# Kernel optimization log

Hardware: AMD Instinct MI355X
Metric: run time of the kernel (lower is better)

## Reference

```python
import jax, jax.numpy as jnp
import numpy as np

L = 2048  # sequence length
V = 2048  # num_tokens == channel width (one-hot embedding)
B = 4     # batch


def _pos_bias(v_table):
    # pos[i,j] = max(i-j, 0); embed via [L,1] table -> [L,L]
    i = jnp.arange(L)
    pos = jnp.maximum(i[:, None] - i[None, :], 0)
    return v_table[pos, 0]


def setup_inputs() -> dict:
    key = jax.random.key(0)
    ks = jax.random.split(key, 11)
    idx = jax.random.randint(ks[0], (B, L), 0, V)
    lin = lambda k, std: (jax.random.normal(k, (V, V), dtype=jnp.float32) * std)
    return {
        "idx": idx,
        # layer_zero: all std=1 (explicit re-init in torch code)
        "Wq0": lin(ks[1], 1.0), "Wk0": lin(ks[2], 1.0), "Wv0": lin(ks[3], 1.0),
        # layer_one: Wk std=1 (re-init), Wv std=0.02 (default init); Wq is zero-fn
        "Wk1": lin(ks[4], 1.0), "Wv1": lin(ks[5], 0.02),
        # layer_two: Wq,Wv std=1 (re-init), Wk std=0.02 (default)
        "Wq2": lin(ks[6], 1.0), "Wk2": lin(ks[7], 0.02), "Wv2": lin(ks[8], 1.0),
        # relative-position embedding tables [L,1], std=0.02
        "v0": jax.random.normal(ks[9], (L, 1), dtype=jnp.float32) * 0.02,
        "v1": jax.random.normal(ks[10], (L, 1), dtype=jnp.float32) * 0.02,
    }


def reference(idx, Wq0, Wk0, Wv0, Wk1, Wv1, Wq2, Wk2, Wv2, v0, v1):
    e = jax.nn.one_hot(idx, V, dtype=jnp.float32)            # [B,L,V]
    tril = jnp.tril(jnp.ones((L, L), dtype=bool))
    p0 = _pos_bias(v0)                                       # [L,L]
    p1 = _pos_bias(v1)

    # layer_zero(e, e): scores = Q@K^T + sum_e(K)[:,None]*pos, tril, @V (no softmax)
    K0 = e @ Wk0.T
    Q0 = e @ Wq0.T
    V0 = e @ Wv0.T
    s0 = jnp.einsum('bqv,bkv->bqk', Q0, K0) + K0.sum(-1)[:, :, None] * p0[None]
    l0 = jnp.where(tril, s0, 0.0) @ V0                       # [B,L,V]

    # layer_one(l0, e): Wq is zero-fn -> only the pos-bias term survives
    K1 = e @ Wk1.T
    V1 = l0 @ Wv1.T
    s1 = K1.sum(-1)[:, :, None] * p1[None]
    l1 = jnp.where(tril, s1, 0.0) @ V1

    # layer_two(e, l1): v is zero-fn -> no pos bias
    K2 = l1 @ Wk2.T
    Q2 = e @ Wq2.T
    V2 = e @ Wv2.T
    s2 = jnp.einsum('bqv,bkv->bqk', Q2, K2)
    logits = jnp.where(tril, s2, 0.0) @ V2                   # [B,L,V]
    return logits
```

## Files before the change

kernel.cpp:

```cpp
#include <hip/hip_runtime.h>

typedef float f32x4 __attribute__((ext_vector_type(4)));
typedef short s16x8 __attribute__((ext_vector_type(8)));

constexpr int L = 2048;
constexpr int V = 2048;
constexpr int NB = 4;
constexpr size_t VV  = (size_t)V * V;
constexpr size_t BLV = (size_t)NB * L * V;
constexpr size_t LV  = (size_t)L * V;

__device__ __forceinline__ unsigned short f2bf(float f) {
    unsigned u = __float_as_uint(f);
    u = (u + 0x7FFFu + ((u >> 16) & 1u)) >> 16;
    return (unsigned short)u;
}
__device__ __forceinline__ float bf2f(unsigned short s) {
    return __uint_as_float(((unsigned)s) << 16);
}

__device__ __forceinline__ void gload16(const unsigned short* g, unsigned short* l) {
    auto gp = (const __attribute__((address_space(1))) unsigned int*)g;
    auto lp = (__attribute__((address_space(3))) unsigned int*)l;
    __builtin_amdgcn_global_load_lds(gp, lp, 16, 0, 0);
}

#define SBAR __builtin_amdgcn_sched_barrier(0)


__device__ __forceinline__ void stage_half(const unsigned short* G, int r0, int k0, int s,
                                           unsigned short* slice, int wave, int lane) {
    int rl = lane >> 2, slot = lane & 3;
    #pragma unroll
    for (int r = 0; r < 2; ++r) {
        int rowl = r * 128 + wave * 16 + rl;
        int colg = k0 + s * 32 + ((slot ^ ((rowl >> 1) & 3)) * 8);
        gload16(G + (size_t)(r0 + rowl) * 2048 + colg,
                slice + (size_t)(r * 128 + wave * 16) * 32);
    }
}

__device__ __forceinline__ s16x8 frag64(const unsigned short* slice, int row, int kc) {
    return *(const s16x8*)&slice[row * 32 + ((kc ^ ((row >> 1) & 3)) * 8)];
}

__device__ __forceinline__ void kloop64(const unsigned short* Ab, const unsigned short* Bb,
                                        int m0, int n0, int NT, unsigned short* lds,
                                        int wave, int lane, int wr, int wc,
                                        f32x4 (&acc)[8][4]) {
    const int r15 = lane & 15, kc = lane >> 4;

    stage_half(Ab, m0, 0, 0, lds + 0,     wave, lane);
    stage_half(Bb, n0, 0, 0, lds + 16384, wave, lane);
    stage_half(Ab, m0, 0, 1, lds + 8192,  wave, lane);
    stage_half(Bb, n0, 0, 1, lds + 24576, wave, lane);
    asm volatile("s_waitcnt vmcnt(4)" ::: "memory");
    SBAR; __builtin_amdgcn_s_barrier(); SBAR;

    for (int t = 0; t < NT; ++t) {
        unsigned short* cur = lds + (t & 1) * 32768;
        unsigned short* nxt = lds + ((t + 1) & 1) * 32768;
        const bool pre = (t + 1 < NT);
        const int k1 = (t + 1) * 64;

        s16x8 b0[4], b1[4], a[4];

        #pragma unroll
        for (int nf = 0; nf < 4; ++nf)
            b0[nf] = frag64(cur + 16384, wc * 64 + nf * 16 + r15, kc);
        #pragma unroll
        for (int mf = 0; mf < 4; ++mf)
            a[mf] = frag64(cur, wr * 128 + mf * 16 + r15, kc);
        if (pre) stage_half(Ab, m0, k1, 0, nxt, wave, lane);
        SBAR; __builtin_amdgcn_s_barrier(); SBAR;
        __builtin_amdgcn_s_setprio(1);
        #pragma unroll
        for (int mf = 0; mf < 4; ++mf)
            #pragma unroll
            for (int nf = 0; nf < 4; ++nf)
                acc[mf][nf] = __builtin_amdgcn_mfma_f32_16x16x32_bf16(a[mf], b0[nf], acc[mf][nf], 0, 0, 0);
        __builtin_amdgcn_s_setprio(0);
        SBAR; __builtin_amdgcn_s_barrier(); SBAR;

        #pragma unroll
        for (int mf = 0; mf < 4; ++mf)
            a[mf] = frag64(cur, wr * 128 + (mf + 4) * 16 + r15, kc);
        if (pre) stage_half(Bb, n0, k1, 0, nxt + 16384, wave, lane);
        SBAR; __builtin_amdgcn_s_barrier(); SBAR;
        __builtin_amdgcn_s_setprio(1);
        #pragma unroll
        for (int mf = 0; mf < 4; ++mf)
            #pragma unroll
            for (int nf = 0; nf < 4; ++nf)
                acc[mf + 4][nf] = __builtin_amdgcn_mfma_f32_16x16x32_bf16(a[mf], b0[nf], acc[mf + 4][nf], 0, 0, 0);
        __builtin_amdgcn_s_setprio(0);
        SBAR;
        if (pre) { asm volatile("s_waitcnt vmcnt(4)" ::: "memory"); }
        else     { asm volatile("s_waitcnt vmcnt(0)" ::: "memory"); }
        SBAR; __builtin_amdgcn_s_barrier(); SBAR;

        #pragma unroll
        for (int nf = 0; nf < 4; ++nf)
            b1[nf] = frag64(cur + 24576, wc * 64 + nf * 16 + r15, kc);
        #pragma unroll
        for (int mf = 0; mf < 4; ++mf)
            a[mf] = frag64(cur + 8192, wr * 128 + mf * 16 + r15, kc);
        if (pre) stage_half(Ab, m0, k1, 1, nxt + 8192, wave, lane);
        SBAR; __builtin_amdgcn_s_barrier(); SBAR;
        __builtin_amdgcn_s_setprio(1);
        #pragma unroll
        for (int mf = 0; mf < 4; ++mf)
            #pragma unroll
            for (int nf = 0; nf < 4; ++nf)
                acc[mf][nf] = __builtin_amdgcn_mfma_f32_16x16x32_bf16(a[mf], b1[nf], acc[mf][nf], 0, 0, 0);
        __builtin_amdgcn_s_setprio(0);
        SBAR; __builtin_amdgcn_s_barrier(); SBAR;

        #pragma unroll
        for (int mf = 0; mf < 4; ++mf)
            a[mf] = frag64(cur + 8192, wr * 128 + (mf + 4) * 16 + r15, kc);
        if (pre) stage_half(Bb, n0, k1, 1, nxt + 24576, wave, lane);
        SBAR; __builtin_amdgcn_s_barrier(); SBAR;
        __builtin_amdgcn_s_setprio(1);
        #pragma unroll
        for (int mf = 0; mf < 4; ++mf)
            #pragma unroll
            for (int nf = 0; nf < 4; ++nf)
                acc[mf + 4][nf] = __builtin_amdgcn_mfma_f32_16x16x32_bf16(a[mf], b1[nf], acc[mf + 4][nf], 0, 0, 0);
        __builtin_amdgcn_s_setprio(0);
        SBAR;
        if (pre) { asm volatile("s_waitcnt vmcnt(4)" ::: "memory"); }
        SBAR; __builtin_amdgcn_s_barrier(); SBAR;
    }
}

template<int OUTM, bool TOEP>
__global__ __launch_bounds__(512, 2) void gemm_big(
    const unsigned short* __restrict__ A, size_t sA,
    const unsigned short* __restrict__ B, size_t sB,
    float* __restrict__ outF, unsigned short* __restrict__ outH, size_t sO,
    const int* __restrict__ idxp, const float* __restrict__ ks)
{
    __shared__ __align__(16) unsigned short lds[2 * 32768];

    const int tid  = threadIdx.x;
    const int lane = tid & 63, wave = tid >> 6;
    const int wr = wave >> 2, wc = wave & 3;
    const int bz = blockIdx.z;
    int bx = blockIdx.x, by = blockIdx.y;
    if constexpr (TOEP) { int tswap = bx; bx = by; by = tswap; }
    const int m0 = by * 256, n0 = bx * 256;
    const int r15 = lane & 15, kc = lane >> 4;

    const unsigned short* Ab = A + (size_t)bz * sA;
    const unsigned short* Bb = B + (size_t)bz * sB;
    const int NT = TOEP ? 4 * (bx + 1) : 32;

    f32x4 acc[8][4];
    const f32x4 zf = {0.f, 0.f, 0.f, 0.f};
    #pragma unroll
    for (int i = 0; i < 8; ++i)
        #pragma unroll
        for (int j = 0; j < 4; ++j) acc[i][j] = zf;

    kloop64(Ab, Bb, m0, n0, NT, lds, wave, lane, wr, wc, acc);

    float csc[4];
    if constexpr (TOEP) {
        #pragma unroll
        for (int nf = 0; nf < 4; ++nf) {
            int gcol = n0 + wc * 64 + nf * 16 + r15;
            csc[nf] = ks[idxp[bz * L + gcol]];
        }
    }
    #pragma unroll
    for (int mf = 0; mf < 8; ++mf) {
        #pragma unroll
        for (int r = 0; r < 4; ++r) {
            int grow = m0 + wr * 128 + mf * 16 + kc * 4 + r;
            #pragma unroll
            for (int nf = 0; nf < 4; ++nf) {
                float v = acc[mf][nf][r];
                if constexpr (TOEP) v *= csc[nf];
                int gcol = n0 + wc * 64 + nf * 16 + r15;
                size_t o = (size_t)bz * sO + (size_t)grow * 2048 + gcol;
                if constexpr (OUTM == 0) outF[o] = v;
                else                     outH[o] = f2bf(v);
            }
        }
    }
}

struct PDesc { const unsigned short* A; const unsigned short* B; float* oF; unsigned short* oH; };

__global__ __launch_bounds__(512, 2) void gemm_pre_big(PDesc d0, PDesc d1, PDesc d2) {
    PDesc d = (blockIdx.z == 0) ? d0 : (blockIdx.z == 1) ? d1 : d2;
    __shared__ __align__(16) unsigned short lds[2 * 32768];

    const int tid  = threadIdx.x;
    const int lane = tid & 63, wave = tid >> 6;
    const int wr = wave >> 2, wc = wave & 3;
    const int m0 = blockIdx.y * 256, n0 = blockIdx.x * 256;
    const int r15 = lane & 15, kc = lane >> 4;

    f32x4 acc[8][4];
    const f32x4 zf = {0.f, 0.f, 0.f, 0.f};
    #pragma unroll
    for (int i = 0; i < 8; ++i)
        #pragma unroll
        for (int j = 0; j < 4; ++j) acc[i][j] = zf;

    kloop64(d.A, d.B, m0, n0, 32, lds, wave, lane, wr, wc, acc);

    const bool isF = (d.oF != nullptr);
    #pragma unroll
    for (int mf = 0; mf < 8; ++mf) {
        #pragma unroll
        for (int r = 0; r < 4; ++r) {
            int grow = m0 + wr * 128 + mf * 16 + kc * 4 + r;
            #pragma unroll
            for (int nf = 0; nf < 4; ++nf) {
                float v = acc[mf][nf][r];
                int gcol = n0 + wc * 64 + nf * 16 + r15;
                size_t o = (size_t)grow * 2048 + gcol;
                if (isF) d.oF[o] = v;
                else     d.oH[o] = f2bf(v);
            }
        }
    }
}

__global__ __launch_bounds__(512, 2) void gemm_preK(const unsigned short* __restrict__ A,
                                                    const unsigned short* __restrict__ B,
                                                    float* __restrict__ outP) {
    __shared__ __align__(16) unsigned short lds[2 * 32768];

    const int tid  = threadIdx.x;
    const int lane = tid & 63, wave = tid >> 6;
    const int wr = wave >> 2, wc = wave & 3;
    const int m0 = blockIdx.y * 256, n0 = blockIdx.x * 256;
    const int r15 = lane & 15, kc = lane >> 4;
    const int z = blockIdx.z;

    const unsigned short* Ab = A + z * 512;
    const unsigned short* Bb = B + z * 512;
    float* outF = outP + (size_t)z * VV;

    f32x4 acc[8][4];
    const f32x4 zf = {0.f, 0.f, 0.f, 0.f};
    #pragma unroll
    for (int i = 0; i < 8; ++i)
        #pragma unroll
        for (int j = 0; j < 4; ++j) acc[i][j] = zf;

    kloop64(Ab, Bb, m0, n0, 8, lds, wave, lane, wr, wc, acc);

    #pragma unroll
    for (int mf = 0; mf < 8; ++mf) {
        #pragma unroll
        for (int r = 0; r < 4; ++r) {
            int grow = m0 + wr * 128 + mf * 16 + kc * 4 + r;
            #pragma unroll
            for (int nf = 0; nf < 4; ++nf) {
                int gcol = n0 + wc * 64 + nf * 16 + r15;
                outF[(size_t)grow * 2048 + gcol] = acc[mf][nf][r];
            }
        }
    }
}

__global__ __launch_bounds__(256) void reduce4_cast(const float* __restrict__ P,
                                                    unsigned short* __restrict__ H) {
    int i = blockIdx.x * 256 + threadIdx.x;
    const float4* p0 = (const float4*)P;
    const float4* p1 = (const float4*)(P + VV);
    const float4* p2 = (const float4*)(P + 2 * VV);
    const float4* p3 = (const float4*)(P + 3 * VV);
    float4 a = p0[i], b = p1[i], c = p2[i], d = p3[i];
    ushort4 h;
    h.x = f2bf(a.x + b.x + c.x + d.x);
    h.y = f2bf(a.y + b.y + c.y + d.y);
    h.z = f2bf(a.z + b.z + c.z + d.z);
    h.w = f2bf(a.w + b.w + c.w + d.w);
    ((ushort4*)H)[i] = h;
}


__global__ __launch_bounds__(256) void colsum_atomic(const float* __restrict__ W,
                                                     float* __restrict__ out) {
    int r0 = blockIdx.x * 8;
    int c = threadIdx.x;
    float s[8];
    #pragma unroll
    for (int i = 0; i < 8; ++i) s[i] = 0.f;
    for (int r = 0; r < 8; ++r) {
        const float* row = W + (size_t)(r0 + r) * V;
        #pragma unroll
        for (int i = 0; i < 8; ++i) s[i] += row[c + i * 256];
    }
    #pragma unroll
    for (int i = 0; i < 8; ++i) atomicAdd(&out[c + i * 256], s[i]);
}

__global__ void init_kernel(float* __restrict__ ks0, float* __restrict__ ks1) {
    int i = blockIdx.x * 256 + threadIdx.x;
    if (i < 2048) { ks0[i] = 0.f; ks1[i] = 0.f; }
}

__global__ __launch_bounds__(256) void tb_fill(const float* __restrict__ v1,
                                               unsigned short* __restrict__ TBh) {
    int n = blockIdx.x;
    int c0 = threadIdx.x * 8;
    s16x8 hv;
    #pragma unroll
    for (int i = 0; i < 8; ++i) {
        int k = c0 + i;
        float f = (k <= n) ? v1[n - k] : 0.f;
        hv[i] = (short)f2bf(f);
    }
    *(s16x8*)&TBh[(size_t)n * 2048 + c0] = hv;
}

struct TDesc { const float* A; unsigned short* Th; };

__global__ void transpose_cast_multi(TDesc d0, TDesc d1, TDesc d2, TDesc d3, TDesc d4) {
    TDesc d;
    switch (blockIdx.z) {
        case 0: d = d0; break;
        case 1: d = d1; break;
        case 2: d = d2; break;
        case 3: d = d3; break;
        default: d = d4; break;
    }
    __shared__ float tile[32][33];
    int x = blockIdx.x * 32 + threadIdx.x;
    int y0 = blockIdx.y * 32;
    for (int r = threadIdx.y; r < 32; r += 8)
        tile[r][threadIdx.x] = d.A[(size_t)(y0 + r) * V + x];
    __syncthreads();
    int xo = blockIdx.y * 32 + threadIdx.x;
    int yo0 = blockIdx.x * 32;
    for (int r = threadIdx.y; r < 32; r += 8)
        d.Th[(size_t)(yo0 + r) * V + xo] = f2bf(tile[threadIdx.x][r]);
}

__global__ __launch_bounds__(256) void cast_kernel(const float* __restrict__ A,
                                                   unsigned short* __restrict__ H,
                                                   int n4) {
    int i = blockIdx.x * 256 + threadIdx.x;
    if (i >= n4) return;
    float4 f = ((const float4*)A)[i];
    ushort4 h;
    h.x = f2bf(f.x); h.y = f2bf(f.y); h.z = f2bf(f.z); h.w = f2bf(f.w);
    ((ushort4*)H)[i] = h;
}


__global__ __launch_bounds__(256) void scatterA_kernel(const int* __restrict__ idx,
                                                       const float* __restrict__ G0,
                                                       const float* __restrict__ ks0,
                                                       const float* __restrict__ v0,
                                                       unsigned short* __restrict__ Th) {
    __shared__ float buck[4 * 2048];
    int tid = threadIdx.x;
    const float4 z4 = make_float4(0.f, 0.f, 0.f, 0.f);
    #pragma unroll
    for (int i = 0; i < 8; ++i) ((float4*)buck)[tid + i * 256] = z4;
    __syncthreads();

    int b = blockIdx.y, q0 = blockIdx.x * 4;
    int qr = tid >> 6, lane = tid & 63;
    int q = q0 + qr;
    const int* idxb = idx + b * L;
    int iq = idxb[q];
    float kq = ks0[iq];
    const float* Grow = G0 + (size_t)iq * V;
    float* brow = buck + qr * 2048;

    int k = lane;
    for (; k + 192 <= q; k += 256) {
        int i0 = idxb[k], i1 = idxb[k + 64], i2 = idxb[k + 128], i3 = idxb[k + 192];
        float g0 = Grow[i0], g1 = Grow[i1], g2 = Grow[i2], g3 = Grow[i3];
        float w0 = v0[q - k], w1 = v0[q - k - 64], w2 = v0[q - k - 128], w3 = v0[q - k - 192];
        atomicAdd(&brow[i0], g0 + kq * w0);
        atomicAdd(&brow[i1], g1 + kq * w1);
        atomicAdd(&brow[i2], g2 + kq * w2);
        atomicAdd(&brow[i3], g3 + kq * w3);
    }
    for (; k <= q; k += 64) {
        int ik = idxb[k];
        atomicAdd(&brow[ik], Grow[ik] + kq * v0[q - k]);
    }
    __syncthreads();
    size_t base = ((size_t)b * L + q0) * V;
    #pragma unroll
    for (int it = 0; it < 4; ++it) {
        int i = tid + it * 256;
        s16x8 hv;
        #pragma unroll
        for (int j = 0; j < 8; ++j) hv[j] = (short)f2bf(buck[i * 8 + j]);
        *(s16x8*)&Th[base + (size_t)i * 8] = hv;
    }
}

__global__ __launch_bounds__(256) void scatterC_kernel(const int* __restrict__ idx,
                                                       const unsigned short* __restrict__ T2h,
                                                       unsigned short* __restrict__ Th) {
    __shared__ float buck[4 * 2048];
    int tid = threadIdx.x;
    const float4 z4 = make_float4(0.f, 0.f, 0.f, 0.f);
    #pragma unroll
    for (int i = 0; i < 8; ++i) ((float4*)buck)[tid + i * 256] = z4;
    __syncthreads();

    int b = blockIdx.y, q0 = blockIdx.x * 4;
    int qr = tid >> 6, lane = tid & 63;
    int q = q0 + qr;
    const int* idxb = idx + b * L;
    int iq = idxb[q];
    const unsigned short* Trow = T2h + ((size_t)b * V + iq) * L;
    float* brow = buck + qr * 2048;

    int k = lane;
    for (; k + 192 <= q; k += 256) {
        int i0 = idxb[k], i1 = idxb[k + 64], i2 = idxb[k + 128], i3 = idxb[k + 192];
        float t0 = bf2f(Trow[k]), t1 = bf2f(Trow[k + 64]);
        float t2 = bf2f(Trow[k + 128]), t3 = bf2f(Trow[k + 192]);
        atomicAdd(&brow[i0], t0);
        atomicAdd(&brow[i1], t1);
        atomicAdd(&brow[i2], t2);
        atomicAdd(&brow[i3], t3);
    }
    for (; k <= q; k += 64)
        atomicAdd(&brow[idxb[k]], bf2f(Trow[k]));
    __syncthreads();
    size_t base = ((size_t)b * L + q0) * V;
    #pragma unroll
    for (int it = 0; it < 4; ++it) {
        int i = tid + it * 256;
        s16x8 hv;
        #pragma unroll
        for (int j = 0; j < 8; ++j) hv[j] = (short)f2bf(buck[i * 8 + j]);
        *(s16x8*)&Th[base + (size_t)i * 8] = hv;
    }
}


extern "C" void kernel_launch(void* const* d_in, const int* in_sizes, int n_in,
                              void* d_out, int out_size, void* d_ws, size_t ws_size,
                              hipStream_t stream) {
    (void)in_sizes; (void)n_in; (void)out_size; (void)ws_size;
    const int*   idx = (const int*)d_in[0];
    const float* Wq0 = (const float*)d_in[1];
    const float* Wk0 = (const float*)d_in[2];
    const float* Wv0 = (const float*)d_in[3];
    const float* Wk1 = (const float*)d_in[4];
    const float* Wv1 = (const float*)d_in[5];
    const float* Wq2 = (const float*)d_in[6];
    const float* Wk2 = (const float*)d_in[7];
    const float* Wv2 = (const float*)d_in[8];
    const float* v0  = (const float*)d_in[9];
    const float* v1  = (const float*)d_in[10];
    float* out = (float*)d_out;

    char* W = (char*)d_ws;
    const size_t MiB = 1024 * 1024;

    unsigned short* PPT = (unsigned short*)W;
    unsigned short* TAh = (unsigned short*)W;
    unsigned short* T2h = (unsigned short*)W;
    float* Rp = (float*)(W + 8 * MiB);
    unsigned short* Y1 = (unsigned short*)(W + 64 * MiB);
    unsigned short* Y2 = (unsigned short*)(W + 72 * MiB);
    unsigned short* Uh  = (unsigned short*)(W + 64 * MiB);
    unsigned short* TCh = Uh;
    float* Gf = (float*)(W + 96 * MiB);
    unsigned short* Y4 = (unsigned short*)(W + 112 * MiB);
    unsigned short* X1 = (unsigned short*)(W + 128 * MiB);
    unsigned short* X2 = (unsigned short*)(W + 136 * MiB);
    unsigned short* X3 = (unsigned short*)(W + 144 * MiB);
    unsigned short* X4 = (unsigned short*)(W + 152 * MiB);
    unsigned short* TBh = X3;
    float* ks0 = (float*)(W + 192 * MiB);
    float* ks1 = (float*)(W + 192 * MiB + 16 * 1024);

    dim3 blk(256);

    {
        TDesc t0{Wq0, X1}, t1{Wk0, X2}, t2{Wq2, X3}, t3{Wk2, X4}, t4{Wv0, Y1};
        transpose_cast_multi<<<dim3(64, 64, 5), dim3(32, 8), 0, stream>>>(t0, t1, t2, t3, t4);
    }
    cast_kernel<<<dim3((int)(VV / 4 / 256)), blk, 0, stream>>>(Wv1, Y2, (int)(VV / 4));
    init_kernel<<<dim3(8), blk, 0, stream>>>(ks0, ks1);
    colsum_atomic<<<dim3(256), blk, 0, stream>>>(Wk0, ks0);
    colsum_atomic<<<dim3(256), blk, 0, stream>>>(Wk1, ks1);

    {
        PDesc dG{X1, X2, Gf, nullptr};
        PDesc dM{X3, X4, nullptr, Y4};
        PDesc dP{Y1, Y2, nullptr, PPT};
        gemm_pre_big<<<dim3(8, 8, 3), dim3(512), 0, stream>>>(dG, dM, dP);
    }
    tb_fill<<<dim3(2048), blk, 0, stream>>>(v1, TBh);
    gemm_preK<<<dim3(8, 8, 4), dim3(512), 0, stream>>>(Y4, PPT, Rp);
    reduce4_cast<<<dim3((int)(VV / 4 / 256)), blk, 0, stream>>>(Rp, X1);

    scatterA_kernel<<<dim3(L / 4, NB), blk, 0, stream>>>(idx, Gf, ks0, v0, TAh);

    gemm_big<1, false><<<dim3(8, 8, NB), dim3(512), 0, stream>>>(
        X1, 0, TAh, LV, nullptr, Uh, LV, nullptr, nullptr);

    gemm_big<1, true><<<dim3(8, 8, NB), dim3(512), 0, stream>>>(
        Uh, LV, TBh, 0, nullptr, T2h, LV, idx, ks1);

    scatterC_kernel<<<dim3(L / 4, NB), blk, 0, stream>>>(idx, T2h, TCh);

    cast_kernel<<<dim3((int)(VV / 4 / 256)), blk, 0, stream>>>(Wv2, X2, (int)(VV / 4));

    gemm_big<0, false><<<dim3(8, 32, 1), dim3(512), 0, stream>>>(
        TCh, 0, X2, 0, out, nullptr, 0, nullptr, nullptr);
}
```

Before: 481.6 us.

## Switch GEMM main loop to triple-buffered 32-wide K stages with one barrier

Replaces the double-buffered 64-wide K-step loop, which had many block barriers per iteration, with a three-slot ring of 32-wide K stages. Loads run two stages ahead and each iteration has a single barrier. LDS per block drops from 128KB to 96KB. The aim is to cut barrier stalls and deepen load/compute overlap, at the cost of twice as many loop iterations with less MFMA work between waits.

```diff
diff --git a/kernel.cpp b/kernel.cpp
--- a/kernel.cpp
+++ b/kernel.cpp
@@ -28,51 +28,52 @@
 #define SBAR __builtin_amdgcn_sched_barrier(0)
 
 
-__device__ __forceinline__ void stage_half(const unsigned short* G, int r0, int k0, int s,
+__device__ __forceinline__ void stage_half(const unsigned short* G, int r0, int k0,
                                            unsigned short* slice, int wave, int lane) {
     int rl = lane >> 2, slot = lane & 3;
     #pragma unroll
     for (int r = 0; r < 2; ++r) {
         int rowl = r * 128 + wave * 16 + rl;
-        int colg = k0 + s * 32 + ((slot ^ ((rowl >> 1) & 3)) * 8);
+        int colg = k0 + ((slot ^ ((rowl >> 1) & 3)) * 8);
         gload16(G + (size_t)(r0 + rowl) * 2048 + colg,
                 slice + (size_t)(r * 128 + wave * 16) * 32);
     }
 }
 
-__device__ __forceinline__ s16x8 frag64(const unsigned short* slice, int row, int kc) {
+__device__ __forceinline__ s16x8 fragx(const unsigned short* slice, int row, int kc) {
     return *(const s16x8*)&slice[row * 32 + ((kc ^ ((row >> 1) & 3)) * 8)];
 }
 
-__device__ __forceinline__ void kloop64(const unsigned short* Ab, const unsigned short* Bb,
+__device__ __forceinline__ void kloop32(const unsigned short* Ab, const unsigned short* Bb,
                                         int m0, int n0, int NT, unsigned short* lds,
                                         int wave, int lane, int wr, int wc,
                                         f32x4 (&acc)[8][4]) {
     const int r15 = lane & 15, kc = lane >> 4;
 
-    stage_half(Ab, m0, 0, 0, lds + 0,     wave, lane);
-    stage_half(Bb, n0, 0, 0, lds + 16384, wave, lane);
-    stage_half(Ab, m0, 0, 1, lds + 8192,  wave, lane);
-    stage_half(Bb, n0, 0, 1, lds + 24576, wave, lane);
+    stage_half(Ab, m0, 0,  lds + 0,     wave, lane);
+    stage_half(Bb, n0, 0,  lds + 8192,  wave, lane);
+    stage_half(Ab, m0, 32, lds + 16384, wave, lane);
+    stage_half(Bb, n0, 32, lds + 24576, wave, lane);
     asm volatile("s_waitcnt vmcnt(4)" ::: "memory");
-    SBAR; __builtin_amdgcn_s_barrier(); SBAR;
-
+    __builtin_amdgcn_s_barrier();
+    SBAR;
+
+    int cb = 0;
     for (int t = 0; t < NT; ++t) {
-        unsigned short* cur = lds + (t & 1) * 32768;
-        unsigned short* nxt = lds + ((t + 1) & 1) * 32768;
-        const bool pre = (t + 1 < NT);
-        const int k1 = (t + 1) * 64;
-
-        s16x8 b0[4], b1[4], a[4];
-
+        const unsigned short* cur = lds + cb * 16384;
+        int sb = cb + 2; if (sb >= 3) sb -= 3;
+        unsigned short* stg = lds + sb * 16384;
+        const bool pre = (t + 2 < NT);
+        const int k2 = (t + 2) * 32;
+
+        s16x8 b0[4], a[4], a2[4];
         #pragma unroll
         for (int nf = 0; nf < 4; ++nf)
-            b0[nf] = frag64(cur + 16384, wc * 64 + nf * 16 + r15, kc);
+            b0[nf] = fragx(cur + 8192, wc * 64 + nf * 16 + r15, kc);
         #pragma unroll
         for (int mf = 0; mf < 4; ++mf)
-            a[mf] = frag64(cur, wr * 128 + mf * 16 + r15, kc);
-        if (pre) stage_half(Ab, m0, k1, 0, nxt, wave, lane);
-        SBAR; __builtin_amdgcn_s_barrier(); SBAR;
+            a[mf] = fragx(cur, wr * 128 + mf * 16 + r15, kc);
+        if (pre) stage_half(Ab, m0, k2, stg, wave, lane);
         __builtin_amdgcn_s_setprio(1);
         #pragma unroll
         for (int mf = 0; mf < 4; ++mf)
@@ -80,57 +81,24 @@
             for (int nf = 0; nf < 4; ++nf)
                 acc[mf][nf] = __builtin_amdgcn_mfma_f32_16x16x32_bf16(a[mf], b0[nf], acc[mf][nf], 0, 0, 0);
         __builtin_amdgcn_s_setprio(0);
-        SBAR; __builtin_amdgcn_s_barrier(); SBAR;
 
         #pragma unroll
         for (int mf = 0; mf < 4; ++mf)
-            a[mf] = frag64(cur, wr * 128 + (mf + 4) * 16 + r15, kc);
-        if (pre) stage_half(Bb, n0, k1, 0, nxt + 16384, wave, lane);
-        SBAR; __builtin_amdgcn_s_barrier(); SBAR;
+            a2[mf] = fragx(cur, wr * 128 + (mf + 4) * 16 + r15, kc);
+        if (pre) stage_half(Bb, n0, k2, stg + 8192, wave, lane);
         __builtin_amdgcn_s_setprio(1);
         #pragma unroll
         for (int mf = 0; mf < 4; ++mf)
             #pragma unroll
             for (int nf = 0; nf < 4; ++nf)
-                acc[mf + 4][nf] = __builtin_amdgcn_mfma_f32_16x16x32_bf16(a[mf], b0[nf], acc[mf + 4][nf], 0, 0, 0);
+                acc[mf + 4][nf] = __builtin_amdgcn_mfma_f32_16x16x32_bf16(a2[mf], b0[nf], acc[mf + 4][nf], 0, 0, 0);
         __builtin_amdgcn_s_setprio(0);
+
+        if (pre)               { asm volatile("s_waitcnt vmcnt(4)" ::: "memory"); }
+        else if (t + 2 == NT)  { asm volatile("s_waitcnt vmcnt(0)" ::: "memory"); }
+        __builtin_amdgcn_s_barrier();
         SBAR;
-        if (pre) { asm volatile("s_waitcnt vmcnt(4)" ::: "memory"); }
-        else     { asm volatile("s_waitcnt vmcnt(0)" ::: "memory"); }
-        SBAR; __builtin_amdgcn_s_barrier(); SBAR;
-
-        #pragma unroll
-        for (int nf = 0; nf < 4; ++nf)
-            b1[nf] = frag64(cur + 24576, wc * 64 + nf * 16 + r15, kc);
-        #pragma unroll
-        for (int mf = 0; mf < 4; ++mf)
-            a[mf] = frag64(cur + 8192, wr * 128 + mf * 16 + r15, kc);
-        if (pre) stage_half(Ab, m0, k1, 1, nxt + 8192, wave, lane);
-        SBAR; __builtin_amdgcn_s_barrier(); SBAR;
-        __builtin_amdgcn_s_setprio(1);
-        #pragma unroll
-        for (int mf = 0; mf < 4; ++mf)
-            #pragma unroll
-            for (int nf = 0; nf < 4; ++nf)
-                acc[mf][nf] = __builtin_amdgcn_mfma_f32_16x16x32_bf16(a[mf], b1[nf], acc[mf][nf], 0, 0, 0);
-        __builtin_amdgcn_s_setprio(0);
-        SBAR; __builtin_amdgcn_s_barrier(); SBAR;
-
-        #pragma unroll
-        for (int mf = 0; mf < 4; ++mf)
-            a[mf] = frag64(cur + 8192, wr * 128 + (mf + 4) * 16 + r15, kc);
-        if (pre) stage_half(Bb, n0, k1, 1, nxt + 24576, wave, lane);
-        SBAR; __builtin_amdgcn_s_barrier(); SBAR;
-        __builtin_amdgcn_s_setprio(1);
-        #pragma unroll
-        for (int mf = 0; mf < 4; ++mf)
-            #pragma unroll
-            for (int nf = 0; nf < 4; ++nf)
-                acc[mf + 4][nf] = __builtin_amdgcn_mfma_f32_16x16x32_bf16(a[mf], b1[nf], acc[mf + 4][nf], 0, 0, 0);
-        __builtin_amdgcn_s_setprio(0);
-        SBAR;
-        if (pre) { asm volatile("s_waitcnt vmcnt(4)" ::: "memory"); }
-        SBAR; __builtin_amdgcn_s_barrier(); SBAR;
+        if (++cb == 3) cb = 0;
     }
 }
 
@@ -141,7 +109,7 @@
     float* __restrict__ outF, unsigned short* __restrict__ outH, size_t sO,
     const int* __restrict__ idxp, const float* __restrict__ ks)
 {
-    __shared__ __align__(16) unsigned short lds[2 * 32768];
+    __shared__ __align__(16) unsigned short lds[3 * 16384];
 
     const int tid  = threadIdx.x;
     const int lane = tid & 63, wave = tid >> 6;
@@ -154,7 +122,7 @@
 
     const unsigned short* Ab = A + (size_t)bz * sA;
     const unsigned short* Bb = B + (size_t)bz * sB;
-    const int NT = TOEP ? 4 * (bx + 1) : 32;
+    const int NT = TOEP ? 8 * (bx + 1) : 64;
 
     f32x4 acc[8][4];
     const f32x4 zf = {0.f, 0.f, 0.f, 0.f};
@@ -163,7 +131,7 @@
         #pragma unroll
         for (int j = 0; j < 4; ++j) acc[i][j] = zf;
 
-    kloop64(Ab, Bb, m0, n0, NT, lds, wave, lane, wr, wc, acc);
+    kloop32(Ab, Bb, m0, n0, NT, lds, wave, lane, wr, wc, acc);
 
     float csc[4];
     if constexpr (TOEP) {
@@ -195,7 +163,7 @@
 
 __global__ __launch_bounds__(512, 2) void gemm_pre_big(PDesc d0, PDesc d1, PDesc d2) {
     PDesc d = (blockIdx.z == 0) ? d0 : (blockIdx.z == 1) ? d1 : d2;
-    __shared__ __align__(16) unsigned short lds[2 * 32768];
+    __shared__ __align__(16) unsigned short lds[3 * 16384];
 
     const int tid  = threadIdx.x;
     const int lane = tid & 63, wave = tid >> 6;
@@ -210,7 +178,7 @@
         #pragma unroll
         for (int j = 0; j < 4; ++j) acc[i][j] = zf;
 
-    kloop64(d.A, d.B, m0, n0, 32, lds, wave, lane, wr, wc, acc);
+    kloop32(d.A, d.B, m0, n0, 64, lds, wave, lane, wr, wc, acc);
 
     const bool isF = (d.oF != nullptr);
     #pragma unroll
@@ -233,7 +201,7 @@
 __global__ __launch_bounds__(512, 2) void gemm_preK(const unsigned short* __restrict__ A,
                                                     const unsigned short* __restrict__ B,
                                                     float* __restrict__ outP) {
-    __shared__ __align__(16) unsigned short lds[2 * 32768];
+    __shared__ __align__(16) unsigned short lds[3 * 16384];
 
     const int tid  = threadIdx.x;
     const int lane = tid & 63, wave = tid >> 6;
@@ -253,7 +221,7 @@
         #pragma unroll
         for (int j = 0; j < 4; ++j) acc[i][j] = zf;
 
-    kloop64(Ab, Bb, m0, n0, 8, lds, wave, lane, wr, wc, acc);
+    kloop32(Ab, Bb, m0, n0, 16, lds, wave, lane, wr, wc, acc);
 
     #pragma unroll
     for (int mf = 0; mf < 8; ++mf) {
```

Result: no change. 473.2 us (-1.7%).
